# Optimization experiments

Hardware: AMD Instinct MI355X
Metric: run time of the kernel (lower is better)

The kernel has to match this reference:

```python
import jax, jax.numpy as jnp
import numpy as np

COST_CLASS = 1.0
COST_POLYLINE = 1.0
COST_DIRECTION = 1.0
EPS = 1e-6


def setup_inputs() -> dict:
    key = jax.random.key(0)
    k1, k2, k3, k4 = jax.random.split(key, 4)
    bs, Q, C, P, T = 2, 256, 16, 20, 256
    return {
        "pred_logits": jax.random.normal(k1, (bs, Q, C), dtype=jnp.float32),
        "pred_polylines": jax.random.normal(k2, (bs, Q, P, 2), dtype=jnp.float32),
        "tgt_labels": jax.random.randint(k3, (T,), 0, C),
        "tgt_polylines": jax.random.normal(k4, (T, P, 2), dtype=jnp.float32),
    }


def reference(pred_logits, pred_polylines, tgt_labels, tgt_polylines):
    # pred_logits: [bs, Q, C]; pred_polylines: [bs, Q, P, 2]
    # tgt_labels: [T]; tgt_polylines: [T, P, 2]
    bs, Q = pred_logits.shape[:2]
    out_prob = jax.nn.softmax(pred_logits.reshape(bs * Q, -1), axis=-1)  # [N, C]
    out_poly = pred_polylines.reshape(bs * Q, *pred_polylines.shape[2:])  # [N, P, 2]

    # classification cost: -p(tgt_class)  -> [N, T]
    cost_class = -out_prob[:, tgt_labels]

    # pairwise polyline L1 cdist, all pairs at once: d[n, t, p, q]
    d = (jnp.abs(out_poly[:, None, :, None, 0] - tgt_polylines[None, :, None, :, 0])
         + jnp.abs(out_poly[:, None, :, None, 1] - tgt_polylines[None, :, None, :, 1]))
    # bidirectional average-of-min distance (Chamfer-style), averaged -> [N, T]
    min1 = d.min(axis=3).mean(axis=2)  # pred -> gt
    min2 = d.min(axis=2).mean(axis=2)  # gt -> pred
    cost_polyline = (min1 + min2) / 2

    # direction cost: 1 - cos(start->end vectors)
    pd = out_poly[:, -1] - out_poly[:, 0]          # [N, 2]
    gd = tgt_polylines[:, -1] - tgt_polylines[:, 0]  # [T, 2]
    pd = pd / (jnp.linalg.norm(pd, axis=-1, keepdims=True) + EPS)
    gd = gd / (jnp.linalg.norm(gd, axis=-1, keepdims=True) + EPS)
    cost_direction = 1.0 - pd @ gd.T               # [N, T]

    C = (COST_CLASS * cost_class
         + COST_POLYLINE * cost_polyline
         + COST_DIRECTION * cost_direction)
    return C.reshape(bs, Q, -1)
```

## Files before the change

### kernel.cpp

```cpp
#include <hip/hip_runtime.h>
#include <math.h>

#define BS   2
#define NQ   256
#define NCLS 16
#define NP   20
#define NT   256
#define NN   (BS * NQ)
#define FEPS 1e-6f
#define PHALF (NP / 2)

__global__ __launch_bounds__(2 * NT) void matcher_cost_kernel(
    const float* __restrict__ logits,
    const float* __restrict__ ppoly,
    const int*   __restrict__ tlabels,
    const float* __restrict__ tpoly,
    float*       __restrict__ out)
{
    const int n   = blockIdx.x;
    const int tid = threadIdx.x;
    const int t   = tid >> 1;
    const int z   = tid & 1;

    __shared__ float s_px[NP];
    __shared__ float s_py[NP];
    __shared__ float s_logit[NCLS];

    if (tid < NP * 2) {
        float v = ppoly[n * NP * 2 + tid];
        if (tid & 1) s_py[tid >> 1] = v;
        else         s_px[tid >> 1] = v;
    }
    if (tid < NCLS) s_logit[tid] = logits[n * NCLS + tid];
    __syncthreads();

    float tx[NP], ty[NP];
    #pragma unroll
    for (int p = 0; p < NP; p += 2) {
        float4 v = *reinterpret_cast<const float4*>(&tpoly[(t * NP + p) * 2]);
        tx[p]     = v.x;  ty[p]     = v.y;
        tx[p + 1] = v.z;  ty[p + 1] = v.w;
    }

    float mx = s_logit[0];
    #pragma unroll
    for (int c = 1; c < NCLS; ++c) mx = fmaxf(mx, s_logit[c]);
    float denom = 0.f;
    #pragma unroll
    for (int c = 0; c < NCLS; ++c) denom += __expf(s_logit[c] - mx);
    const int lbl = tlabels[t];
    const float cost_class = -__expf(s_logit[lbl] - mx) / denom;

    float m2[NP];
    #pragma unroll
    for (int q = 0; q < NP; ++q) m2[q] = 1e30f;

    float sum1 = 0.f;
    const int p0 = z * PHALF;
    #pragma unroll
    for (int pp = 0; pp < PHALF; ++pp) {
        const float px = s_px[p0 + pp];
        const float py = s_py[p0 + pp];
        float m1 = 1e30f;
        #pragma unroll
        for (int q = 0; q < NP; ++q) {
            const float d = fabsf(px - tx[q]) + fabsf(py - ty[q]);
            m1    = fminf(m1, d);
            m2[q] = fminf(m2[q], d);
        }
        sum1 += m1;
    }
    sum1 += __shfl_xor(sum1, 1);
    float sum2 = 0.f;
    #pragma unroll
    for (int q = 0; q < NP; ++q)
        sum2 += fminf(m2[q], __shfl_xor(m2[q], 1));

    const float cost_poly = (sum1 + sum2) * (0.5f / (float)NP);

    float pdx = s_px[NP - 1] - s_px[0];
    float pdy = s_py[NP - 1] - s_py[0];
    const float pn = sqrtf(pdx * pdx + pdy * pdy) + FEPS;
    pdx /= pn; pdy /= pn;

    float gdx = tx[NP - 1] - tx[0];
    float gdy = ty[NP - 1] - ty[0];
    const float gn = sqrtf(gdx * gdx + gdy * gdy) + FEPS;
    gdx /= gn; gdy /= gn;

    const float cost_dir = 1.f - (pdx * gdx + pdy * gdy);

    if (z == 0) out[n * NT + t] = cost_class + cost_poly + cost_dir;
}

extern "C" void kernel_launch(void* const* d_in, const int* in_sizes, int n_in,
                              void* d_out, int out_size, void* d_ws, size_t ws_size,
                              hipStream_t stream) {
    const float* logits  = (const float*)d_in[0];
    const float* ppoly   = (const float*)d_in[1];
    const int*   tlabels = (const int*)d_in[2];
    const float* tpoly   = (const float*)d_in[3];
    float*       out     = (float*)d_out;

    matcher_cost_kernel<<<dim3(NN), dim3(2 * NT), 0, stream>>>(
        logits, ppoly, tlabels, tpoly, out);
}
```

Before: 12.45 us.

## Split each target across four lanes over its points and shrink blocks

Each (pred, target) pair is now handled by four lanes, each owning five target points, instead of two lanes each owning half of the pred points. The per-pred minimum is reduced with two xor shuffles per pred point. Blocks are 256 threads covering 64 targets, giving four times as many blocks. Softmax exponentials are computed once per block into shared memory rather than in every thread. The aim is to cut per-thread register pressure (5-entry arrays instead of 20) and raise occupancy, at the cost of 40 shuffles per thread, redundant per-block setup, and extra global loads for the direction endpoints.

```diff
diff --git a/kernel.cpp b/kernel.cpp
--- a/kernel.cpp
+++ b/kernel.cpp
@@ -1,30 +1,34 @@
 #include <hip/hip_runtime.h>
 #include <math.h>
 
-#define BS   2
-#define NQ   256
-#define NCLS 16
-#define NP   20
-#define NT   256
-#define NN   (BS * NQ)
-#define FEPS 1e-6f
-#define PHALF (NP / 2)
+#define BS    2
+#define NQ    256
+#define NCLS  16
+#define NP    20
+#define NT    256
+#define NN    (BS * NQ)
+#define FEPS  1e-6f
+#define QPL   5
+#define TPB   64
+#define THREADS 256
 
-__global__ __launch_bounds__(2 * NT) void matcher_cost_kernel(
+__global__ __launch_bounds__(THREADS, 8) void matcher_cost_kernel(
     const float* __restrict__ logits,
     const float* __restrict__ ppoly,
     const int*   __restrict__ tlabels,
     const float* __restrict__ tpoly,
     float*       __restrict__ out)
 {
-    const int n   = blockIdx.x;
-    const int tid = threadIdx.x;
-    const int t   = tid >> 1;
-    const int z   = tid & 1;
+    const int bid   = blockIdx.x;
+    const int n     = bid >> 2;
+    const int tbase = (bid & 3) * TPB;
+    const int tid   = threadIdx.x;
+    const int t     = tbase + (tid >> 2);
+    const int z     = tid & 3;
 
-    __shared__ float s_px[NP];
-    __shared__ float s_py[NP];
+    __shared__ float s_px[NP], s_py[NP];
     __shared__ float s_logit[NCLS];
+    __shared__ float s_prob[NCLS];
 
     if (tid < NP * 2) {
         float v = ppoly[n * NP * 2 + tid];
@@ -34,57 +38,63 @@
     if (tid < NCLS) s_logit[tid] = logits[n * NCLS + tid];
     __syncthreads();
 
-    float tx[NP], ty[NP];
+    if (tid < NCLS) {
+        float mx = s_logit[0];
+        #pragma unroll
+        for (int c = 1; c < NCLS; ++c) mx = fmaxf(mx, s_logit[c]);
+        s_prob[tid] = __expf(s_logit[tid] - mx);
+    }
+    __syncthreads();
+
+    float tx[QPL], ty[QPL], m2[QPL];
+    const float* tp = &tpoly[(t * NP + z * QPL) * 2];
     #pragma unroll
-    for (int p = 0; p < NP; p += 2) {
-        float4 v = *reinterpret_cast<const float4*>(&tpoly[(t * NP + p) * 2]);
-        tx[p]     = v.x;  ty[p]     = v.y;
-        tx[p + 1] = v.z;  ty[p + 1] = v.w;
+    for (int k = 0; k < QPL; ++k) {
+        float2 v = *reinterpret_cast<const float2*>(&tp[2 * k]);
+        tx[k] = v.x; ty[k] = v.y; m2[k] = 1e30f;
     }
 
-    float mx = s_logit[0];
+    float sum1 = 0.f;
     #pragma unroll
-    for (int c = 1; c < NCLS; ++c) mx = fmaxf(mx, s_logit[c]);
+    for (int p = 0; p < NP; ++p) {
+        const float px = s_px[p];
+        const float py = s_py[p];
+        float d0 = fabsf(px - tx[0]) + fabsf(py - ty[0]);
+        float d1 = fabsf(px - tx[1]) + fabsf(py - ty[1]);
+        float d2 = fabsf(px - tx[2]) + fabsf(py - ty[2]);
+        float d3 = fabsf(px - tx[3]) + fabsf(py - ty[3]);
+        float d4 = fabsf(px - tx[4]) + fabsf(py - ty[4]);
+        m2[0] = fminf(m2[0], d0);
+        m2[1] = fminf(m2[1], d1);
+        m2[2] = fminf(m2[2], d2);
+        m2[3] = fminf(m2[3], d3);
+        m2[4] = fminf(m2[4], d4);
+        float m1 = fminf(fminf(fminf(d0, d1), fminf(d2, d3)), d4);
+        m1 = fminf(m1, __shfl_xor(m1, 1));
+        m1 = fminf(m1, __shfl_xor(m1, 2));
+        sum1 += m1;
+    }
+    float sum2 = ((m2[0] + m2[1]) + (m2[2] + m2[3])) + m2[4];
+    sum2 += __shfl_xor(sum2, 1);
+    sum2 += __shfl_xor(sum2, 2);
+
+    const float cost_poly = (sum1 + sum2) * (0.5f / (float)NP);
+
     float denom = 0.f;
     #pragma unroll
-    for (int c = 0; c < NCLS; ++c) denom += __expf(s_logit[c] - mx);
+    for (int c = 0; c < NCLS; ++c) denom += s_prob[c];
     const int lbl = tlabels[t];
-    const float cost_class = -__expf(s_logit[lbl] - mx) / denom;
-
-    float m2[NP];
-    #pragma unroll
-    for (int q = 0; q < NP; ++q) m2[q] = 1e30f;
-
-    float sum1 = 0.f;
-    const int p0 = z * PHALF;
-    #pragma unroll
-    for (int pp = 0; pp < PHALF; ++pp) {
-        const float px = s_px[p0 + pp];
-        const float py = s_py[p0 + pp];
-        float m1 = 1e30f;
-        #pragma unroll
-        for (int q = 0; q < NP; ++q) {
-            const float d = fabsf(px - tx[q]) + fabsf(py - ty[q]);
-            m1    = fminf(m1, d);
-            m2[q] = fminf(m2[q], d);
-        }
-        sum1 += m1;
-    }
-    sum1 += __shfl_xor(sum1, 1);
-    float sum2 = 0.f;
-    #pragma unroll
-    for (int q = 0; q < NP; ++q)
-        sum2 += fminf(m2[q], __shfl_xor(m2[q], 1));
-
-    const float cost_poly = (sum1 + sum2) * (0.5f / (float)NP);
+    const float cost_class = -s_prob[lbl] / denom;
 
     float pdx = s_px[NP - 1] - s_px[0];
     float pdy = s_py[NP - 1] - s_py[0];
     const float pn = sqrtf(pdx * pdx + pdy * pdy) + FEPS;
     pdx /= pn; pdy /= pn;
 
-    float gdx = tx[NP - 1] - tx[0];
-    float gdy = ty[NP - 1] - ty[0];
+    float2 g0 = *reinterpret_cast<const float2*>(&tpoly[t * NP * 2]);
+    float2 g1 = *reinterpret_cast<const float2*>(&tpoly[(t * NP + NP - 1) * 2]);
+    float gdx = g1.x - g0.x;
+    float gdy = g1.y - g0.y;
     const float gn = sqrtf(gdx * gdx + gdy * gdy) + FEPS;
     gdx /= gn; gdy /= gn;
 
@@ -102,6 +112,6 @@
     const float* tpoly   = (const float*)d_in[3];
     float*       out     = (float*)d_out;
 
-    matcher_cost_kernel<<<dim3(NN), dim3(2 * NT), 0, stream>>>(
+    matcher_cost_kernel<<<dim3(NN * (NT / TPB)), dim3(THREADS), 0, stream>>>(
         logits, ppoly, tlabels, tpoly, out);
 }
```

Result: slower. 16.75 us (+34.5%).
